# Performance work log

Hardware: AMD Instinct MI355X
Metric: run time of the kernel (lower is better)

Reference implementation:

```python
import jax, jax.numpy as jnp
import numpy as np


def setup_inputs() -> dict:
    key = jax.random.key(0)
    k1, k2 = jax.random.split(key)
    inp = jax.random.normal(k1, (16, 64, 64, 64), dtype=jnp.float32)  # (B, D, H, W)
    codebook = jax.random.normal(k2, (1024, 64), dtype=jnp.float32)  # (K, D)
    return {"input": inp, "codebook": codebook}


def reference(input, codebook):
    # input: (B, D, *spatial); codebook: (K, D)
    B, D = input.shape[0], input.shape[1]
    spatial = input.shape[2:]
    # move channel dim last, flatten to tokens: (N, D)
    x = jnp.moveaxis(input, 1, -1).reshape(-1, D)
    # squared L2 distances (cdist^2), computed via expansion to avoid (N,K,D)
    x_sq = jnp.sum(x * x, axis=-1, keepdims=True)            # (N, 1)
    e_sq = jnp.sum(codebook * codebook, axis=-1)             # (K,)
    dist = x_sq - 2.0 * (x @ codebook.T) + e_sq              # (N, K)
    idx = jnp.argmin(dist, axis=-1)                          # (N,)
    quantized = jnp.take(codebook, idx, axis=0)              # (N, D)
    # reshape back to (B, *spatial, D) then move D to axis 1
    out = jnp.moveaxis(quantized.reshape((B,) + spatial + (D,)), -1, 1)
    indices = idx.reshape((B,) + spatial)
    return out, indices
```

## Files before the change

kernel.cpp:

```cpp
#include <hip/hip_runtime.h>


typedef _Float16 v8h  __attribute__((ext_vector_type(8)));
typedef float    v16f __attribute__((ext_vector_type(16)));

constexpr int   D         = 64;
constexpr int   K         = 1024;
constexpr int   HW        = 4096;
constexpr int   DHW       = D * HW;
constexpr int   OUT_ELEMS = 16 * DHW;
constexpr float EPS       = 1e-3f;


__global__ __launch_bounds__(256) void vq_prep(
    const float* __restrict__ cb, _Float16* __restrict__ CH, float* __restrict__ esq)
{
    const int blk = blockIdx.x, tid = threadIdx.x;
    if (blk < 72) {
        const int gid  = blk * 256 + tid;
        const int lane = gid & 63;
        const int fid  = gid >> 6;
        const int t    = fid / 9;
        const int kc   = fid - 9 * t;
        const int l31  = lane & 31;
        const int lh   = lane >> 5;
        const int cw   = t * 32 + l31;
        v8h h;
        if (kc < 8) {
            const int  kk = kc & 3;
            const bool lo = kc >= 4;
            const float* src = cb + cw * D + kk * 16 + lh * 8;
            #pragma unroll
            for (int j = 0; j < 8; ++j) {
                const float v = -2.0f * src[j];
                const _Float16 vh = (_Float16)v;
                h[j] = lo ? (_Float16)(v - (float)vh) : vh;
            }
        } else {
            #pragma unroll
            for (int j = 0; j < 8; ++j) h[j] = (_Float16)0.0f;
            if (lh == 0) {
                const float4* c4 = (const float4*)(cb + cw * D);
                float a0 = 0.f, a1 = 0.f, a2 = 0.f, a3 = 0.f;
                #pragma unroll
                for (int j = 0; j < 16; ++j) {
                    const float4 c = c4[j];
                    a0 = fmaf(c.x, c.x, a0);
                    a1 = fmaf(c.y, c.y, a1);
                    a2 = fmaf(c.z, c.z, a2);
                    a3 = fmaf(c.w, c.w, a3);
                }
                const float e = (a0 + a1) + (a2 + a3);
                const _Float16 ehi = (_Float16)e;
                h[0] = ehi;
                h[1] = (_Float16)(e - (float)ehi);
            }
        }
        *(v8h*)(CH + (size_t)fid * 512 + lane * 8) = h;
    } else {
        const int cw = (blk - 72) * 256 + tid;
        const float4* c4 = (const float4*)(cb + cw * D);
        float a0 = 0.f, a1 = 0.f, a2 = 0.f, a3 = 0.f;
        #pragma unroll
        for (int j = 0; j < 16; ++j) {
            const float4 c = c4[j];
            a0 = fmaf(c.x, c.x, a0);
            a1 = fmaf(c.y, c.y, a1);
            a2 = fmaf(c.z, c.z, a2);
            a3 = fmaf(c.w, c.w, a3);
        }
        esq[cw] = (a0 + a1) + (a2 + a3);
    }
}

__global__ __launch_bounds__(256, 3) void vq_scan(
    const float* __restrict__ input,
    const float* __restrict__ codebook,
    const _Float16* __restrict__ CH,
    const float* __restrict__ esq,
    float* __restrict__ out)
{
    __shared__ _Float16 s_bf[2][2][4][64][8];
    __shared__ float    s_esq[K];
    __shared__ float    s_pv[4][64];
    __shared__ float    s_p2[4][64];
    __shared__ int      s_pk[4][64];
    __shared__ int      s_idx[64];
    __shared__ int      s_list[64];
    __shared__ int      s_cnt;
    __shared__ float    s_xf[64];
    __shared__ float    s_redv[4];
    __shared__ int      s_redk[4];
    __shared__ float    s_q[64][65];

    const int tid  = threadIdx.x;
    const int lane = tid & 63;
    const int q    = __builtin_amdgcn_readfirstlane(tid >> 6);
    const int lh   = lane >> 5;
    const int tok0 = blockIdx.x * 64;
    const int b    = tok0 >> 12;
    const int hwb  = tok0 & 4095;

    if (tid == 0) s_cnt = 0;

    *(float4*)&s_esq[tid * 4] = *(const float4*)&esq[tid * 4];

    {
        const float* xb = input + (size_t)b * DHW + hwb;
        #pragma unroll
        for (int pass = 0; pass < 4; ++pass) {
            const int d   = pass * 16 + (tid >> 4);
            const int hw4 = (tid & 15) * 4;
            const float4 v = *(const float4*)(xb + (size_t)d * HW + hw4);
            const float vv[4] = {v.x, v.y, v.z, v.w};
            #pragma unroll
            for (int u = 0; u < 4; ++u) {
                const int tk = hw4 + u;
                const float f = vv[u];
                const _Float16 fh = (_Float16)f;
                s_bf[0][tk >> 5][d >> 4][((d >> 3) & 1) * 32 + (tk & 31)][d & 7] = fh;
                s_bf[1][tk >> 5][d >> 4][((d >> 3) & 1) * 32 + (tk & 31)][d & 7] =
                    (_Float16)(f - (float)fh);
            }
        }
    }
    __syncthreads();

    v8h bh[2][4], bl[2][4];
    #pragma unroll
    for (int ct = 0; ct < 2; ++ct)
        #pragma unroll
        for (int kc = 0; kc < 4; ++kc) {
            bh[ct][kc] = *(const v8h*)&s_bf[0][ct][kc][lane][0];
            bl[ct][kc] = *(const v8h*)&s_bf[1][ct][kc][lane][0];
        }

    v8h b5;
    #pragma unroll
    for (int j = 0; j < 8; ++j) b5[j] = (_Float16)0.0f;
    if (lh == 0) { b5[0] = (_Float16)1.0f; b5[1] = (_Float16)1.0f; }

    v16f Z = {0,0,0,0,0,0,0,0,0,0,0,0,0,0,0,0};
    const float INF = __builtin_huge_valf();
    float bv0 = INF, b20 = INF, bv1 = INF, b21 = INF;
    int   sl0 = 0, sl1 = 0;

    const v8h* Abase = (const v8h*)CH + lane;

    #pragma unroll 2
    for (int t = 0; t < 8; ++t) {
        const v8h* Ap = Abase + (size_t)((q * 8 + t) * 9) * 64;
        const v8h ah0 = Ap[0],   ah1 = Ap[64],  ah2 = Ap[128], ah3 = Ap[192];
        const v8h al0 = Ap[256], al1 = Ap[320], al2 = Ap[384], al3 = Ap[448];
        const v8h ae  = Ap[512];

        v16f acc0 = __builtin_amdgcn_mfma_f32_32x32x16_f16(ae, b5, Z, 0, 0, 0);
        v16f acc1 = __builtin_amdgcn_mfma_f32_32x32x16_f16(ae, b5, Z, 0, 0, 0);

        acc0 = __builtin_amdgcn_mfma_f32_32x32x16_f16(ah0, bh[0][0], acc0, 0, 0, 0);
        acc1 = __builtin_amdgcn_mfma_f32_32x32x16_f16(ah0, bh[1][0], acc1, 0, 0, 0);
        acc0 = __builtin_amdgcn_mfma_f32_32x32x16_f16(ah1, bh[0][1], acc0, 0, 0, 0);
        acc1 = __builtin_amdgcn_mfma_f32_32x32x16_f16(ah1, bh[1][1], acc1, 0, 0, 0);
        acc0 = __builtin_amdgcn_mfma_f32_32x32x16_f16(ah2, bh[0][2], acc0, 0, 0, 0);
        acc1 = __builtin_amdgcn_mfma_f32_32x32x16_f16(ah2, bh[1][2], acc1, 0, 0, 0);
        acc0 = __builtin_amdgcn_mfma_f32_32x32x16_f16(ah3, bh[0][3], acc0, 0, 0, 0);
        acc1 = __builtin_amdgcn_mfma_f32_32x32x16_f16(ah3, bh[1][3], acc1, 0, 0, 0);

        acc0 = __builtin_amdgcn_mfma_f32_32x32x16_f16(ah0, bl[0][0], acc0, 0, 0, 0);
        acc1 = __builtin_amdgcn_mfma_f32_32x32x16_f16(ah0, bl[1][0], acc1, 0, 0, 0);
        acc0 = __builtin_amdgcn_mfma_f32_32x32x16_f16(ah1, bl[0][1], acc0, 0, 0, 0);
        acc1 = __builtin_amdgcn_mfma_f32_32x32x16_f16(ah1, bl[1][1], acc1, 0, 0, 0);
        acc0 = __builtin_amdgcn_mfma_f32_32x32x16_f16(ah2, bl[0][2], acc0, 0, 0, 0);
        acc1 = __builtin_amdgcn_mfma_f32_32x32x16_f16(ah2, bl[1][2], acc1, 0, 0, 0);
        acc0 = __builtin_amdgcn_mfma_f32_32x32x16_f16(ah3, bl[0][3], acc0, 0, 0, 0);
        acc1 = __builtin_amdgcn_mfma_f32_32x32x16_f16(ah3, bl[1][3], acc1, 0, 0, 0);

        acc0 = __builtin_amdgcn_mfma_f32_32x32x16_f16(al0, bh[0][0], acc0, 0, 0, 0);
        acc1 = __builtin_amdgcn_mfma_f32_32x32x16_f16(al0, bh[1][0], acc1, 0, 0, 0);
        acc0 = __builtin_amdgcn_mfma_f32_32x32x16_f16(al1, bh[0][1], acc0, 0, 0, 0);
        acc1 = __builtin_amdgcn_mfma_f32_32x32x16_f16(al1, bh[1][1], acc1, 0, 0, 0);
        acc0 = __builtin_amdgcn_mfma_f32_32x32x16_f16(al2, bh[0][2], acc0, 0, 0, 0);
        acc1 = __builtin_amdgcn_mfma_f32_32x32x16_f16(al2, bh[1][2], acc1, 0, 0, 0);
        acc0 = __builtin_amdgcn_mfma_f32_32x32x16_f16(al3, bh[0][3], acc0, 0, 0, 0);
        acc1 = __builtin_amdgcn_mfma_f32_32x32x16_f16(al3, bh[1][3], acc1, 0, 0, 0);

        #pragma unroll
        for (int r = 0; r < 16; ++r) {
            const int slot = (t << 4) | r;
            const float s0 = acc0[r];
            b20 = __builtin_amdgcn_fmed3f(s0, bv0, b20);
            if (s0 < bv0) { bv0 = s0; sl0 = slot; }
            const float s1 = acc1[r];
            b21 = __builtin_amdgcn_fmed3f(s1, bv1, b21);
            if (s1 < bv1) { bv1 = s1; sl1 = slot; }
        }
    }

    #pragma unroll
    for (int ct = 0; ct < 2; ++ct) {
        const float bv = ct ? bv1 : bv0;
        const float b2 = ct ? b21 : b20;
        const int   sl = ct ? sl1 : sl0;
        const float obv = __shfl_xor(bv, 32, 64);
        const float ob2 = __shfl_xor(b2, 32, 64);
        const int   osl = __shfl_xor(sl, 32, 64);
        const bool  oth = obv < bv;
        const float B1  = oth ? obv : bv;
        const float B2  = fminf(fmaxf(bv, obv), fminf(b2, ob2));
        const int   wsl = oth ? osl : sl;
        const int   wlh = oth ? (lh ^ 1) : lh;
        const int   r   = wsl & 15;
        const int   tt  = wsl >> 4;
        const int   cw  = (q * 8 + tt) * 32 + (r & 3) + 8 * (r >> 2) + 4 * wlh;
        if (lane < 32) {
            s_pv[q][ct * 32 + lane] = B1;
            s_p2[q][ct * 32 + lane] = B2;
            s_pk[q][ct * 32 + lane] = cw;
        }
    }
    __syncthreads();

    if (tid < 64) {
        float B1 = INF, B2 = INF; int CW = 0;
        #pragma unroll
        for (int qq = 0; qq < 4; ++qq) {
            const float pv = s_pv[qq][tid];
            const float p2 = s_p2[qq][tid];
            const int   pk = s_pk[qq][tid];
            if (pv < B1) { B2 = fminf(B1, p2); B1 = pv; CW = pk; }
            else         { B2 = fminf(B2, pv); }
        }
        s_idx[tid] = CW;
        if (B2 - B1 < EPS) {
            const int p = atomicAdd(&s_cnt, 1);
            s_list[p] = tid;
        }
    }
    __syncthreads();

    {
        const int cnt = s_cnt;
        const int rr  = tid >> 2;
        const int c   = tid & 3;
        for (int ii = 0; ii < cnt; ++ii) {
            const int tl = s_list[ii];
            if (tid < 64) s_xf[tid] = input[(size_t)b * DHW + (size_t)tid * HW + (hwb + tl)];
            __syncthreads();
            const float4* xs4 = (const float4*)&s_xf[c * 16];
            const float4 x0 = xs4[0], x1 = xs4[1], x2 = xs4[2], x3 = xs4[3];
            float bestv = INF; int bestk = K;
            #pragma unroll 4
            for (int i = 0; i < 16; ++i) {
                const int k = i * 64 + rr;
                const float4* c4 = (const float4*)(codebook + (size_t)k * D + c * 16);
                const float4 c0 = c4[0], c1 = c4[1], c2 = c4[2], c3 = c4[3];
                float p0 = 0.f, p1 = 0.f, p2 = 0.f, p3 = 0.f;
                p0 = fmaf(x0.x, c0.x, p0); p0 = fmaf(x0.y, c0.y, p0);
                p0 = fmaf(x0.z, c0.z, p0); p0 = fmaf(x0.w, c0.w, p0);
                p1 = fmaf(x1.x, c1.x, p1); p1 = fmaf(x1.y, c1.y, p1);
                p1 = fmaf(x1.z, c1.z, p1); p1 = fmaf(x1.w, c1.w, p1);
                p2 = fmaf(x2.x, c2.x, p2); p2 = fmaf(x2.y, c2.y, p2);
                p2 = fmaf(x2.z, c2.z, p2); p2 = fmaf(x2.w, c2.w, p2);
                p3 = fmaf(x3.x, c3.x, p3); p3 = fmaf(x3.y, c3.y, p3);
                p3 = fmaf(x3.z, c3.z, p3); p3 = fmaf(x3.w, c3.w, p3);
                float dp = (p0 + p1) + (p2 + p3);
                dp += __shfl_xor(dp, 1, 64);
                dp += __shfl_xor(dp, 2, 64);
                const float s = fmaf(-2.0f, dp, s_esq[k]);
                if (s < bestv) { bestv = s; bestk = k; }
            }
            #pragma unroll
            for (int off = 4; off <= 32; off <<= 1) {
                const float ov = __shfl_xor(bestv, off, 64);
                const int   ok = __shfl_xor(bestk, off, 64);
                if (ov < bestv || (ov == bestv && ok < bestk)) { bestv = ov; bestk = ok; }
            }
            if (lane == 0) { s_redv[q] = bestv; s_redk[q] = bestk; }
            __syncthreads();
            if (tid == 0) {
                float bb = s_redv[0]; int bk = s_redk[0];
                #pragma unroll
                for (int w = 1; w < 4; ++w) {
                    const float v = s_redv[w]; const int kk = s_redk[w];
                    if (v < bb || (v == bb && kk < bk)) { bb = v; bk = kk; }
                }
                s_idx[tl] = bk;
            }
            __syncthreads();
        }
    }

    {
        const int rs  = tid >> 2;
        const int c   = tid & 3;
        const int idx = s_idx[rs];
        const float4* src = (const float4*)(codebook + (size_t)idx * D + c * 16);
        #pragma unroll
        for (int j = 0; j < 4; ++j) {
            const float4 v = src[j];
            float* dst = &s_q[rs][c * 16 + j * 4];
            dst[0] = v.x; dst[1] = v.y; dst[2] = v.z; dst[3] = v.w;
        }
    }
    __syncthreads();
    {
        float* ob = out + (size_t)b * DHW + hwb;
        #pragma unroll
        for (int pass = 0; pass < 4; ++pass) {
            const int d   = pass * 16 + (tid >> 4);
            const int hw4 = (tid & 15) * 4;
            float4 v;
            v.x = s_q[hw4 + 0][d];
            v.y = s_q[hw4 + 1][d];
            v.z = s_q[hw4 + 2][d];
            v.w = s_q[hw4 + 3][d];
            *(float4*)(ob + (size_t)d * HW + hw4) = v;
        }
        if (tid < 64) out[OUT_ELEMS + tok0 + tid] = (float)s_idx[tid];
    }
}

extern "C" void kernel_launch(void* const* d_in, const int* in_sizes, int n_in,
                              void* d_out, int out_size, void* d_ws, size_t ws_size,
                              hipStream_t stream) {
    const float* input    = (const float*)d_in[0];
    const float* codebook = (const float*)d_in[1];
    float* out            = (float*)d_out;

    _Float16* CH  = (_Float16*)d_ws;
    float*    esq = (float*)((char*)d_ws + 294912);

    vq_prep<<<76, 256, 0, stream>>>(codebook, CH, esq);
    vq_scan<<<1024, 256, 0, stream>>>(input, codebook, CH, esq, out);
}
```

Before: 105.4 us.

## Raise occupancy by overlapping LDS buffers and streaming low-half B from LDS

Merges the fp16 split-input buffer and the quantized-output staging buffer into one shared union and drops the shared copy of codebook norms, reading them from global memory instead. The low-half B fragments are now reloaded from LDS inside the scan loop rather than held in registers, and the loop is no longer unrolled. Together these cut LDS and VGPR use so launch bounds can request 4 blocks per CU. The cost is extra LDS traffic in the hot loop and less instruction-level parallelism.

```diff
diff --git a/kernel.cpp b/kernel.cpp
--- a/kernel.cpp
+++ b/kernel.cpp
@@ -73,15 +73,17 @@
     }
 }
 
-__global__ __launch_bounds__(256, 3) void vq_scan(
+__global__ __launch_bounds__(256, 4) void vq_scan(
     const float* __restrict__ input,
     const float* __restrict__ codebook,
     const _Float16* __restrict__ CH,
     const float* __restrict__ esq,
     float* __restrict__ out)
 {
-    __shared__ _Float16 s_bf[2][2][4][64][8];
-    __shared__ float    s_esq[K];
+    __shared__ union {
+        _Float16 bf[2][2][4][64][8];
+        float    q[64][65];
+    } u;
     __shared__ float    s_pv[4][64];
     __shared__ float    s_p2[4][64];
     __shared__ int      s_pk[4][64];
@@ -91,7 +93,6 @@
     __shared__ float    s_xf[64];
     __shared__ float    s_redv[4];
     __shared__ int      s_redk[4];
-    __shared__ float    s_q[64][65];
 
     const int tid  = threadIdx.x;
     const int lane = tid & 63;
@@ -103,8 +104,6 @@
 
     if (tid == 0) s_cnt = 0;
 
-    *(float4*)&s_esq[tid * 4] = *(const float4*)&esq[tid * 4];
-
     {
         const float* xb = input + (size_t)b * DHW + hwb;
         #pragma unroll
@@ -114,26 +113,24 @@
             const float4 v = *(const float4*)(xb + (size_t)d * HW + hw4);
             const float vv[4] = {v.x, v.y, v.z, v.w};
             #pragma unroll
-            for (int u = 0; u < 4; ++u) {
-                const int tk = hw4 + u;
-                const float f = vv[u];
+            for (int uu = 0; uu < 4; ++uu) {
+                const int tk = hw4 + uu;
+                const float f = vv[uu];
                 const _Float16 fh = (_Float16)f;
-                s_bf[0][tk >> 5][d >> 4][((d >> 3) & 1) * 32 + (tk & 31)][d & 7] = fh;
-                s_bf[1][tk >> 5][d >> 4][((d >> 3) & 1) * 32 + (tk & 31)][d & 7] =
+                u.bf[0][tk >> 5][d >> 4][((d >> 3) & 1) * 32 + (tk & 31)][d & 7] = fh;
+                u.bf[1][tk >> 5][d >> 4][((d >> 3) & 1) * 32 + (tk & 31)][d & 7] =
                     (_Float16)(f - (float)fh);
             }
         }
     }
     __syncthreads();
 
-    v8h bh[2][4], bl[2][4];
+    v8h bh[2][4];
     #pragma unroll
     for (int ct = 0; ct < 2; ++ct)
         #pragma unroll
-        for (int kc = 0; kc < 4; ++kc) {
-            bh[ct][kc] = *(const v8h*)&s_bf[0][ct][kc][lane][0];
-            bl[ct][kc] = *(const v8h*)&s_bf[1][ct][kc][lane][0];
-        }
+        for (int kc = 0; kc < 4; ++kc)
+            bh[ct][kc] = *(const v8h*)&u.bf[0][ct][kc][lane][0];
 
     v8h b5;
     #pragma unroll
@@ -147,42 +144,37 @@
 
     const v8h* Abase = (const v8h*)CH + lane;
 
-    #pragma unroll 2
+    #pragma unroll 1
     for (int t = 0; t < 8; ++t) {
         const v8h* Ap = Abase + (size_t)((q * 8 + t) * 9) * 64;
-        const v8h ah0 = Ap[0],   ah1 = Ap[64],  ah2 = Ap[128], ah3 = Ap[192];
-        const v8h al0 = Ap[256], al1 = Ap[320], al2 = Ap[384], al3 = Ap[448];
-        const v8h ae  = Ap[512];
+        v8h ah[4], al[4];
+        #pragma unroll
+        for (int kc = 0; kc < 4; ++kc) {
+            ah[kc] = Ap[kc * 64];
+            al[kc] = Ap[(kc + 4) * 64];
+        }
+        const v8h ae = Ap[512];
 
         v16f acc0 = __builtin_amdgcn_mfma_f32_32x32x16_f16(ae, b5, Z, 0, 0, 0);
         v16f acc1 = __builtin_amdgcn_mfma_f32_32x32x16_f16(ae, b5, Z, 0, 0, 0);
 
-        acc0 = __builtin_amdgcn_mfma_f32_32x32x16_f16(ah0, bh[0][0], acc0, 0, 0, 0);
-        acc1 = __builtin_amdgcn_mfma_f32_32x32x16_f16(ah0, bh[1][0], acc1, 0, 0, 0);
-        acc0 = __builtin_amdgcn_mfma_f32_32x32x16_f16(ah1, bh[0][1], acc0, 0, 0, 0);
-        acc1 = __builtin_amdgcn_mfma_f32_32x32x16_f16(ah1, bh[1][1], acc1, 0, 0, 0);
-        acc0 = __builtin_amdgcn_mfma_f32_32x32x16_f16(ah2, bh[0][2], acc0, 0, 0, 0);
-        acc1 = __builtin_amdgcn_mfma_f32_32x32x16_f16(ah2, bh[1][2], acc1, 0, 0, 0);
-        acc0 = __builtin_amdgcn_mfma_f32_32x32x16_f16(ah3, bh[0][3], acc0, 0, 0, 0);
-        acc1 = __builtin_amdgcn_mfma_f32_32x32x16_f16(ah3, bh[1][3], acc1, 0, 0, 0);
-
-        acc0 = __builtin_amdgcn_mfma_f32_32x32x16_f16(ah0, bl[0][0], acc0, 0, 0, 0);
-        acc1 = __builtin_amdgcn_mfma_f32_32x32x16_f16(ah0, bl[1][0], acc1, 0, 0, 0);
-        acc0 = __builtin_amdgcn_mfma_f32_32x32x16_f16(ah1, bl[0][1], acc0, 0, 0, 0);
-        acc1 = __builtin_amdgcn_mfma_f32_32x32x16_f16(ah1, bl[1][1], acc1, 0, 0, 0);
-        acc0 = __builtin_amdgcn_mfma_f32_32x32x16_f16(ah2, bl[0][2], acc0, 0, 0, 0);
-        acc1 = __builtin_amdgcn_mfma_f32_32x32x16_f16(ah2, bl[1][2], acc1, 0, 0, 0);
-        acc0 = __builtin_amdgcn_mfma_f32_32x32x16_f16(ah3, bl[0][3], acc0, 0, 0, 0);
-        acc1 = __builtin_amdgcn_mfma_f32_32x32x16_f16(ah3, bl[1][3], acc1, 0, 0, 0);
-
-        acc0 = __builtin_amdgcn_mfma_f32_32x32x16_f16(al0, bh[0][0], acc0, 0, 0, 0);
-        acc1 = __builtin_amdgcn_mfma_f32_32x32x16_f16(al0, bh[1][0], acc1, 0, 0, 0);
-        acc0 = __builtin_amdgcn_mfma_f32_32x32x16_f16(al1, bh[0][1], acc0, 0, 0, 0);
-        acc1 = __builtin_amdgcn_mfma_f32_32x32x16_f16(al1, bh[1][1], acc1, 0, 0, 0);
-        acc0 = __builtin_amdgcn_mfma_f32_32x32x16_f16(al2, bh[0][2], acc0, 0, 0, 0);
-        acc1 = __builtin_amdgcn_mfma_f32_32x32x16_f16(al2, bh[1][2], acc1, 0, 0, 0);
-        acc0 = __builtin_amdgcn_mfma_f32_32x32x16_f16(al3, bh[0][3], acc0, 0, 0, 0);
-        acc1 = __builtin_amdgcn_mfma_f32_32x32x16_f16(al3, bh[1][3], acc1, 0, 0, 0);
+        #pragma unroll
+        for (int kc = 0; kc < 4; ++kc) {
+            acc0 = __builtin_amdgcn_mfma_f32_32x32x16_f16(ah[kc], bh[0][kc], acc0, 0, 0, 0);
+            acc1 = __builtin_amdgcn_mfma_f32_32x32x16_f16(ah[kc], bh[1][kc], acc1, 0, 0, 0);
+        }
+        #pragma unroll
+        for (int kc = 0; kc < 4; ++kc) {
+            acc0 = __builtin_amdgcn_mfma_f32_32x32x16_f16(al[kc], bh[0][kc], acc0, 0, 0, 0);
+            acc1 = __builtin_amdgcn_mfma_f32_32x32x16_f16(al[kc], bh[1][kc], acc1, 0, 0, 0);
+        }
+        #pragma unroll
+        for (int kc = 0; kc < 4; ++kc) {
+            const v8h bl0 = *(const v8h*)&u.bf[1][0][kc][lane][0];
+            const v8h bl1 = *(const v8h*)&u.bf[1][1][kc][lane][0];
+            acc0 = __builtin_amdgcn_mfma_f32_32x32x16_f16(ah[kc], bl0, acc0, 0, 0, 0);
+            acc1 = __builtin_amdgcn_mfma_f32_32x32x16_f16(ah[kc], bl1, acc1, 0, 0, 0);
+        }
 
         #pragma unroll
         for (int r = 0; r < 16; ++r) {
@@ -266,7 +258,7 @@
                 float dp = (p0 + p1) + (p2 + p3);
                 dp += __shfl_xor(dp, 1, 64);
                 dp += __shfl_xor(dp, 2, 64);
-                const float s = fmaf(-2.0f, dp, s_esq[k]);
+                const float s = fmaf(-2.0f, dp, esq[k]);
                 if (s < bestv) { bestv = s; bestk = k; }
             }
             #pragma unroll
@@ -298,7 +290,7 @@
         #pragma unroll
         for (int j = 0; j < 4; ++j) {
             const float4 v = src[j];
-            float* dst = &s_q[rs][c * 16 + j * 4];
+            float* dst = &u.q[rs][c * 16 + j * 4];
             dst[0] = v.x; dst[1] = v.y; dst[2] = v.z; dst[3] = v.w;
         }
     }
@@ -310,10 +302,10 @@
             const int d   = pass * 16 + (tid >> 4);
             const int hw4 = (tid & 15) * 4;
             float4 v;
-            v.x = s_q[hw4 + 0][d];
-            v.y = s_q[hw4 + 1][d];
-            v.z = s_q[hw4 + 2][d];
-            v.w = s_q[hw4 + 3][d];
+            v.x = u.q[hw4 + 0][d];
+            v.y = u.q[hw4 + 1][d];
+            v.z = u.q[hw4 + 2][d];
+            v.w = u.q[hw4 + 3][d];
             *(float4*)(ob + (size_t)d * HW + hw4) = v;
         }
         if (tid < 64) out[OUT_ELEMS + tok0 + tid] = (float)s_idx[tid];
```

Measured after the change: 108.7 us. 3.1% more time.
